# Performance work log

Hardware: AMD Instinct MI355X
Metric: run time of the kernel (lower is better)

The kernel has to match this reference:

```python
import jax, jax.numpy as jnp
import numpy as np

# Spiking boolean gates on {0,1}-valued floats:
#   AND(a,b) = a*b ; OR(a,b) = a + b - a*b ; NOT(a) = 1 - a
#   XOR(a,b) = a + b - 2*a*b ; FullAdder: s = a^b^c, carry = a*b + c*(a^b)

def _xor(a, b):
    return a + b - 2.0 * a * b

def _or(a, b):
    return a + b - a * b


def setup_inputs() -> dict:
    key = jax.random.key(0)
    # FP64 bit patterns as 0/1 spikes; batch of 2M words -> 512 MB input
    x = jax.random.randint(key, (2_000_000, 64), 0, 2).astype(jnp.float32)
    return {"x": x}


def reference(x):
    ones = jnp.ones(x.shape[:-1] + (1,), x.dtype)
    # exponent bits (big-endian) -> little-endian
    e_le = jnp.flip(x[..., 1:12], axis=-1)  # [..., 11]
    # constant 1023 little-endian = ten 1s then a 0; NOT of it
    not_1023 = [0.0] * 10 + [1.0]
    # shift = e - 1023 via e + ~1023 + 1 (initial carry = 1)
    s_bits = []
    carry = ones
    for i in range(11):
        a = e_le[..., i:i + 1]
        b = not_1023[i]
        axb = _xor(a, b)
        s = _xor(axb, carry)
        carry = a * b + carry * axb
        s_bits.append(s)
    s_inv = [1.0 - s for s in s_bits]
    # high bits 3..10 all zero
    hi_zero = s_inv[3]
    for i in range(4, 11):
        hi_zero = hi_zero * s_inv[i]
    is_s = [
        hi_zero * (s_inv[0] * (s_inv[1] * s_inv[2])),   # shift == 0
        hi_zero * (s_bits[0] * (s_inv[1] * s_inv[2])),  # shift == 1
        hi_zero * (s_inv[0] * (s_bits[1] * s_inv[2])),  # shift == 2
        hi_zero * (s_bits[0] * (s_bits[1] * s_inv[2])), # shift == 3
        hi_zero * (s_inv[0] * (s_inv[1] * s_bits[2])),  # shift == 4
        hi_zero * (s_bits[0] * (s_inv[1] * s_bits[2])), # shift == 5
    ]
    m = [x[..., 12 + i:13 + i] for i in range(6)]  # top mantissa bits
    final_bits = []
    for b in range(6):
        terms = []
        for s in range(6):
            if s == b:
                terms.append(is_s[s] * ones)
            elif s > b and s - 1 - b < 6:
                terms.append(is_s[s] * m[s - 1 - b])
        res = terms[0]
        for t in terms[1:]:
            res = _or(res, t)
        final_bits.append(res)
    return jnp.concatenate(list(reversed(final_bits)), axis=-1)
```

## Files before the change

### kernel.cpp

```cpp
#include <hip/hip_runtime.h>

__global__ __launch_bounds__(256) void extract_low6_kernel(
    const float* __restrict__ x, float* __restrict__ out, int nrows) {
    int r = blockIdx.x * blockDim.x + threadIdx.x;
    if (r >= nrows) return;

    const float* row = x + (size_t)r * 64;
    float4 f0 = *(const float4*)(row);
    float4 f1 = *(const float4*)(row + 4);
    float4 f2 = *(const float4*)(row + 8);
    float4 f3 = *(const float4*)(row + 12);
    float2 f4 = *(const float2*)(row + 16);

    int e = 0;
    e |= (int)(f0.y != 0.f) << 10;
    e |= (int)(f0.z != 0.f) << 9;
    e |= (int)(f0.w != 0.f) << 8;
    e |= (int)(f1.x != 0.f) << 7;
    e |= (int)(f1.y != 0.f) << 6;
    e |= (int)(f1.z != 0.f) << 5;
    e |= (int)(f1.w != 0.f) << 4;
    e |= (int)(f2.x != 0.f) << 3;
    e |= (int)(f2.y != 0.f) << 2;
    e |= (int)(f2.z != 0.f) << 1;
    e |= (int)(f2.w != 0.f);

    int mant = 0;
    mant |= (int)(f3.x != 0.f) << 5;
    mant |= (int)(f3.y != 0.f) << 4;
    mant |= (int)(f3.z != 0.f) << 3;
    mant |= (int)(f3.w != 0.f) << 2;
    mant |= (int)(f4.x != 0.f) << 1;
    mant |= (int)(f4.y != 0.f);

    unsigned d = (unsigned)(e - 1023) & 2047u;
    int low6 = (d <= 5u) ? (((0x40 | mant) << d) >> 6) & 63 : 0;

    float2* o = (float2*)(out + (size_t)r * 6);
    o[0] = make_float2((float)((low6 >> 5) & 1), (float)((low6 >> 4) & 1));
    o[1] = make_float2((float)((low6 >> 3) & 1), (float)((low6 >> 2) & 1));
    o[2] = make_float2((float)((low6 >> 1) & 1), (float)(low6 & 1));
}

extern "C" void kernel_launch(void* const* d_in, const int* in_sizes, int n_in,
                              void* d_out, int out_size, void* d_ws, size_t ws_size,
                              hipStream_t stream) {
    const float* x = (const float*)d_in[0];
    float* out = (float*)d_out;
    int nrows = in_sizes[0] / 64;
    int block = 256;
    int grid = (nrows + block - 1) / block;
    extract_low6_kernel<<<grid, block, 0, stream>>>(x, out, nrows);
}
```

Measured before the change: 606.1 us.

## Stage row loads and output stores through shared memory for coalescing

Threads now load each row's first 20 floats cooperatively, so consecutive lanes read consecutive float4s within a row instead of striding 256 bytes apart. The data goes into padded shared memory, is decoded per row, and the six output floats per row are written back as contiguous float2 chunks. Bit tests now read bit 23 of the float representation instead of comparing against zero. This aims to improve DRAM access efficiency at the cost of extra LDS traffic and two barriers per block.

```diff
diff --git a/kernel.cpp b/kernel.cpp
--- a/kernel.cpp
+++ b/kernel.cpp
@@ -1,45 +1,60 @@
 #include <hip/hip_runtime.h>
+
+
+#define ROWS 256
+#define STR  21
 
 __global__ __launch_bounds__(256) void extract_low6_kernel(
     const float* __restrict__ x, float* __restrict__ out, int nrows) {
-    int r = blockIdx.x * blockDim.x + threadIdx.x;
-    if (r >= nrows) return;
+    __shared__ float sin_[ROWS * STR];
+    __shared__ float sout[ROWS * 6];
 
-    const float* row = x + (size_t)r * 64;
-    float4 f0 = *(const float4*)(row);
-    float4 f1 = *(const float4*)(row + 4);
-    float4 f2 = *(const float4*)(row + 8);
-    float4 f3 = *(const float4*)(row + 12);
-    float2 f4 = *(const float2*)(row + 16);
+    const int t = threadIdx.x;
+    const int rowBase = blockIdx.x * ROWS;
+    int rem = nrows - rowBase;
+    if (rem > ROWS) rem = ROWS;
 
-    int e = 0;
-    e |= (int)(f0.y != 0.f) << 10;
-    e |= (int)(f0.z != 0.f) << 9;
-    e |= (int)(f0.w != 0.f) << 8;
-    e |= (int)(f1.x != 0.f) << 7;
-    e |= (int)(f1.y != 0.f) << 6;
-    e |= (int)(f1.z != 0.f) << 5;
-    e |= (int)(f1.w != 0.f) << 4;
-    e |= (int)(f2.x != 0.f) << 3;
-    e |= (int)(f2.y != 0.f) << 2;
-    e |= (int)(f2.z != 0.f) << 1;
-    e |= (int)(f2.w != 0.f);
+    const float* gbase = x + (size_t)rowBase * 64;
+    #pragma unroll
+    for (int k = 0; k < 5; ++k) {
+        int idx  = k * 256 + t;
+        int row  = idx / 5;
+        int quad = idx - row * 5;
+        if (row < rem) {
+            float4 v = *(const float4*)(gbase + row * 64 + quad * 4);
+            float* d = &sin_[row * STR + quad * 4];
+            d[0] = v.x; d[1] = v.y; d[2] = v.z; d[3] = v.w;
+        }
+    }
+    __syncthreads();
 
-    int mant = 0;
-    mant |= (int)(f3.x != 0.f) << 5;
-    mant |= (int)(f3.y != 0.f) << 4;
-    mant |= (int)(f3.z != 0.f) << 3;
-    mant |= (int)(f3.w != 0.f) << 2;
-    mant |= (int)(f4.x != 0.f) << 1;
-    mant |= (int)(f4.y != 0.f);
+    if (t < rem) {
+        const float* s = &sin_[t * STR];
+        int e = 0;
+        #pragma unroll
+        for (int i = 0; i < 11; ++i)
+            e |= (int)((__float_as_uint(s[1 + i]) >> 23) & 1u) << (10 - i);
+        int mant = 0;
+        #pragma unroll
+        for (int i = 0; i < 6; ++i)
+            mant |= (int)((__float_as_uint(s[12 + i]) >> 23) & 1u) << (5 - i);
+        unsigned d = (unsigned)(e - 1023) & 2047u;
+        int low6 = (d <= 5u) ? (((0x40 | mant) << d) >> 6) & 63 : 0;
+        float* o = &sout[t * 6];
+        #pragma unroll
+        for (int j = 0; j < 6; ++j)
+            o[j] = (float)((low6 >> (5 - j)) & 1);
+    }
+    __syncthreads();
 
-    unsigned d = (unsigned)(e - 1023) & 2047u;
-    int low6 = (d <= 5u) ? (((0x40 | mant) << d) >> 6) & 63 : 0;
-
-    float2* o = (float2*)(out + (size_t)r * 6);
-    o[0] = make_float2((float)((low6 >> 5) & 1), (float)((low6 >> 4) & 1));
-    o[1] = make_float2((float)((low6 >> 3) & 1), (float)((low6 >> 2) & 1));
-    o[2] = make_float2((float)((low6 >> 1) & 1), (float)(low6 & 1));
+    float* obase = out + (size_t)rowBase * 6;
+    const int nw = rem * 6;
+    #pragma unroll
+    for (int k = 0; k < 3; ++k) {
+        int idx = k * 256 + t;
+        if (idx * 2 < nw)
+            *(float2*)(obase + idx * 2) = *(float2*)(&sout[idx * 2]);
+    }
 }
 
 extern "C" void kernel_launch(void* const* d_in, const int* in_sizes, int n_in,
@@ -48,7 +63,6 @@
     const float* x = (const float*)d_in[0];
     float* out = (float*)d_out;
     int nrows = in_sizes[0] / 64;
-    int block = 256;
-    int grid = (nrows + block - 1) / block;
-    extract_low6_kernel<<<grid, block, 0, stream>>>(x, out, nrows);
+    int grid = (nrows + ROWS - 1) / ROWS;
+    extract_low6_kernel<<<grid, 256, 0, stream>>>(x, out, nrows);
 }
```

After: 609.6 us. No clear change (+0.6%).
